# Optimization experiments

Measured on AMD Instinct MI355X. Metric: run time of the kernel, lower is better.

Reference implementation:

```python
import jax, jax.numpy as jnp
import numpy as np

K = 5      # unfold kernel size
S = 2      # unfold stride
EPS = 1e-6


def _extract_patches(feature):
    # torch nn.Unfold(kernel=(5,5), stride=2) -> [b, c*25, L], channel-major then
    # row-major kernel offsets; reproduced here with 25 strided slices.
    b, c, h, w = feature.shape
    oh = (h - K) // S + 1
    ow = (w - K) // S + 1
    slices = [feature[:, :, i:i + S * (oh - 1) + 1:S, j:j + S * (ow - 1) + 1:S]
              for i in range(K) for j in range(K)]
    patches = jnp.stack(slices, axis=2)                # [b, c, 25, oh, ow]
    patches = patches.reshape(b, c, K * K, oh * ow)    # [b, c, 25, L]
    return patches.transpose(0, 3, 2, 1)               # [b, L, 25, c]


def setup_inputs() -> dict:
    key = jax.random.key(0)
    k1, k2 = jax.random.split(key)
    feature = jax.random.normal(k1, (32, 128, 63, 63), dtype=jnp.float32)
    label = jax.random.randint(k2, (32,), 0, 2).astype(jnp.int32)
    return {"feature": feature, "label": label}


def reference(feature, label):
    patch = _extract_patches(feature)                  # [b, L, 25, c]
    norms = jnp.linalg.norm(patch, axis=-1)            # [b, L, 25]
    dots = jnp.einsum('blpc,blqc->blpq', patch, patch)  # [b, L, 25, 25]
    # torch cosine_similarity: dot / max(||x||*||y||, eps)
    denom = jnp.maximum(norms[..., :, None] * norms[..., None, :], EPS)
    cos = 1.0 - dots / denom                           # [b, L, 25, 25]
    s = jnp.mean(cos, axis=-1)                         # [b, L, 25]
    m = jnp.max(s, axis=-1)                            # [b, L]
    # topk(k=1) over L then mean over the k dim == max over L
    top = jnp.max(m, axis=-1)                          # [b]
    fake_mask = label.astype(top.dtype)
    real_mask = (1 - label).astype(top.dtype)
    real_loss = jnp.sum(top * real_mask) / jnp.sum(real_mask)
    fake_loss = jnp.sum(top * fake_mask) / jnp.sum(fake_mask)
    loss = 1.0 - fake_loss + real_loss
    return jnp.maximum(loss, 0.0)
```

## Files before the change

kernel.cpp:

```cpp
#include <hip/hip_runtime.h>

#define NB 32
#define NC 128
#define NH 63
#define NW 63
#define HW 3969
#define OH 30
#define SEGW 19
#define NROW 9
#define POSN (NROW*SEGW)
#define NSST 10
#define NSEG 4
#define NBLK (NB*NSST*NSEG)

typedef _Float16 half2_t __attribute__((ext_vector_type(2)));
__device__ __forceinline__ half2_t u2h(unsigned u) { return __builtin_bit_cast(half2_t, u); }
__device__ __forceinline__ unsigned h2u(half2_t h) { return __builtin_bit_cast(unsigned, h); }

__device__ __forceinline__ float dot2(unsigned a, unsigned b, float c) {
#if __has_builtin(__builtin_amdgcn_fdot2)
    return __builtin_amdgcn_fdot2(u2h(a), u2h(b), c, false);
#else
    const half2_t x = u2h(a), y = u2h(b);
    c = fmaf((float)x[0], (float)y[0], c);
    return fmaf((float)x[1], (float)y[1], c);
#endif
}

__device__ __forceinline__ unsigned pk16(float a, float b) {
#if __has_builtin(__builtin_amdgcn_cvt_pkrtz)
    return __builtin_bit_cast(unsigned, __builtin_amdgcn_cvt_pkrtz(a, b));
#else
    const half2_t h = {(_Float16)a, (_Float16)b};
    return h2u(h);
#endif
}

__global__ __launch_bounds__(256) void seg_fused(const float* __restrict__ f,
                                                 float* __restrict__ slots) {
    const int lb  = (blockIdx.x & 7) * (NBLK / 8) + (blockIdx.x >> 3);
    const int b   = lb / (NSST * NSEG);
    const int rem = lb % (NSST * NSEG);
    const int sst = rem >> 2, g = rem & 3;
    const int y0 = 6 * sst, xlo = 16 * g;
    const int t = threadIdx.x;

    __shared__ unsigned band[POSN * 64];
    __shared__ float sinv[POSN];
    __shared__ unsigned sinvh[POSN];
    __shared__ uint4 Slh[16][24];
    __shared__ float wmax[3][4];

    if (t < POSN) {
        const int r = t / SEGW, xx = t % SEGW;
        const int x = xlo + xx;
        float inv = 0.0f;
        if (x < NW) {
            const float* gp = f + (size_t)b * NC * HW + (size_t)(y0 + r) * NW + x;
            float ss = 0.0f;
            float vc[16], vn[16];
            #pragma unroll
            for (int k = 0; k < 16; ++k) vc[k] = gp[(size_t)k * HW];
            #pragma unroll
            for (int ch = 0; ch < 8; ++ch) {
                if (ch < 7) {
                    #pragma unroll
                    for (int k = 0; k < 16; ++k)
                        vn[k] = gp[(size_t)((ch + 1) * 16 + k) * HW];
                }
                #pragma unroll
                for (int k = 0; k < 16; ++k) ss = fmaf(vc[k], vc[k], ss);
                unsigned u[8];
                #pragma unroll
                for (int j = 0; j < 8; ++j) u[j] = pk16(vc[2 * j], vc[2 * j + 1]);
                *(uint4*)&band[t * 64 + (((2 * ch     + t) & 15) << 2)] =
                    make_uint4(u[0], u[1], u[2], u[3]);
                *(uint4*)&band[t * 64 + (((2 * ch + 1 + t) & 15) << 2)] =
                    make_uint4(u[4], u[5], u[6], u[7]);
                #pragma unroll
                for (int k = 0; k < 16; ++k) vc[k] = vn[k];
            }
            inv = (ss > 0.0f) ? rsqrtf(ss) : 0.0f;
        } else {
            #pragma unroll
            for (int j = 0; j < 16; ++j)
                *(uint4*)&band[t * 64 + (((j + t) & 15) << 2)] = make_uint4(0u, 0u, 0u, 0u);
        }
        sinv[t] = inv;
        const half2_t i2 = {(_Float16)inv, (_Float16)inv};
        sinvh[t] = h2u(i2);
    }
    __syncthreads();

    #pragma unroll
    for (int jj = 0; jj < 2; ++jj) {
        const int i = t + jj * 256;
        if (i < 384) {
            const int tl = i >> 4, slot = i & 15;
            const int s_ = tl >> 3, txx = tl & 7;
            half2_t s0 = u2h(0u), s1 = u2h(0u), s2 = u2h(0u), s3 = u2h(0u);
            #pragma unroll
            for (int pr = 0; pr < 5; ++pr)
                #pragma unroll
                for (int pc = 0; pc < 5; ++pc) {
                    const int pos = (2 * s_ + pr) * SEGW + 2 * txx + pc;
                    const uint4 v = *(const uint4*)&band[pos * 64 + (((slot + pos) & 15) << 2)];
                    const half2_t iv = u2h(sinvh[pos]);
                    s0 = u2h(v.x) * iv + s0;
                    s1 = u2h(v.y) * iv + s1;
                    s2 = u2h(v.z) * iv + s2;
                    s3 = u2h(v.w) * iv + s3;
                }
            Slh[slot][tl] = make_uint4(h2u(s0), h2u(s1), h2u(s2), h2u(s3));
        }
    }
    __syncthreads();

    float m[3] = {0.0f, 0.0f, 0.0f};
    if (t < 200) {
        const int txx = t / 25, p = t % 25;
        if (8 * g + txx < OH) {
            const int pos0 = (p / 5) * SEGW + 2 * txx + (p % 5);
            #pragma unroll
            for (int j = 0; j < 3; ++j) {
                const int pos = pos0 + 2 * SEGW * j;
                const int tl  = 8 * j + txx;
                float acc = 0.0f;
                #pragma unroll
                for (int slot = 0; slot < 16; ++slot) {
                    const uint4 sv = Slh[slot][tl];
                    const uint4 v  = *(const uint4*)&band[pos * 64 + (((slot + pos) & 15) << 2)];
                    acc = dot2(v.x, sv.x, acc);
                    acc = dot2(v.y, sv.y, acc);
                    acc = dot2(v.z, sv.z, acc);
                    acc = dot2(v.w, sv.w, acc);
                }
                m[j] = fmaxf(0.0f, 1.0f - acc * sinv[pos] * 0.04f);
            }
        }
    }
    #pragma unroll
    for (int off = 1; off < 64; off <<= 1) {
        m[0] = fmaxf(m[0], __shfl_xor(m[0], off));
        m[1] = fmaxf(m[1], __shfl_xor(m[1], off));
        m[2] = fmaxf(m[2], __shfl_xor(m[2], off));
    }
    if ((t & 63) == 0) {
        wmax[0][t >> 6] = m[0];
        wmax[1][t >> 6] = m[1];
        wmax[2][t >> 6] = m[2];
    }
    __syncthreads();
    if (t < 3) {
        const float mm = fmaxf(fmaxf(wmax[t][0], wmax[t][1]),
                               fmaxf(wmax[t][2], wmax[t][3]));
        slots[((b * OH) + 3 * sst + t) * 4 + g] = mm;
    }
}

__global__ __launch_bounds__(128) void finalize(const float* __restrict__ slots,
                                                const int* __restrict__ label,
                                                float* __restrict__ out) {
    const int t = threadIdx.x;
    __shared__ float bmax[32];
    const int b = t >> 2, j = t & 3;
    float m = 0.0f;
    for (int i = j; i < 120; i += 4) m = fmaxf(m, slots[b * 120 + i]);
    m = fmaxf(m, __shfl_xor(m, 1));
    m = fmaxf(m, __shfl_xor(m, 2));
    if (j == 0) bmax[b] = m;
    __syncthreads();
    if (t == 0) {
        float fs = 0.0f, rs = 0.0f, fc = 0.0f, rc = 0.0f;
        for (int b2 = 0; b2 < NB; ++b2) {
            const float tb  = bmax[b2];
            const float lbv = (float)label[b2];
            fs += tb * lbv;          fc += lbv;
            rs += tb * (1.0f - lbv); rc += (1.0f - lbv);
        }
        const float loss = 1.0f - fs / fc + rs / rc;
        out[0] = fmaxf(loss, 0.0f);
    }
}

extern "C" void kernel_launch(void* const* d_in, const int* in_sizes, int n_in,
                              void* d_out, int out_size, void* d_ws, size_t ws_size,
                              hipStream_t stream) {
    const float* feature = (const float*)d_in[0];
    const int* label     = (const int*)d_in[1];
    float* out   = (float*)d_out;
    float* slots = (float*)d_ws;

    seg_fused<<<NBLK, 256, 0, stream>>>(feature, slots);
    finalize<<<1, 128, 0, stream>>>(slots, label, out);
}
```

Before: 33.05 us.

## Retile into square 13x13 pixel blocks covering 5x5 output windows

```diff
diff --git a/kernel.cpp b/kernel.cpp
--- a/kernel.cpp
+++ b/kernel.cpp
@@ -6,12 +6,12 @@
 #define NW 63
 #define HW 3969
 #define OH 30
-#define SEGW 19
-#define NROW 9
+#define SEGW 13
+#define NROW 13
 #define POSN (NROW*SEGW)
-#define NSST 10
-#define NSEG 4
-#define NBLK (NB*NSST*NSEG)
+#define NSST 6
+#define NCS 6
+#define NBLK (NB*NSST*NCS)
 
 typedef _Float16 half2_t __attribute__((ext_vector_type(2)));
 __device__ __forceinline__ half2_t u2h(unsigned u) { return __builtin_bit_cast(half2_t, u); }
@@ -39,53 +39,45 @@
 __global__ __launch_bounds__(256) void seg_fused(const float* __restrict__ f,
                                                  float* __restrict__ slots) {
     const int lb  = (blockIdx.x & 7) * (NBLK / 8) + (blockIdx.x >> 3);
-    const int b   = lb / (NSST * NSEG);
-    const int rem = lb % (NSST * NSEG);
-    const int sst = rem >> 2, g = rem & 3;
-    const int y0 = 6 * sst, xlo = 16 * g;
+    const int b   = lb / (NSST * NCS);
+    const int rem = lb % (NSST * NCS);
+    const int sst = rem / NCS, cs = rem % NCS;
+    const int y0 = 10 * sst, xlo = 10 * cs;
     const int t = threadIdx.x;
 
     __shared__ unsigned band[POSN * 64];
     __shared__ float sinv[POSN];
     __shared__ unsigned sinvh[POSN];
-    __shared__ uint4 Slh[16][24];
-    __shared__ float wmax[3][4];
+    __shared__ uint4 Slh[16][25];
+    __shared__ float wmax[4];
 
     if (t < POSN) {
         const int r = t / SEGW, xx = t % SEGW;
-        const int x = xlo + xx;
-        float inv = 0.0f;
-        if (x < NW) {
-            const float* gp = f + (size_t)b * NC * HW + (size_t)(y0 + r) * NW + x;
-            float ss = 0.0f;
-            float vc[16], vn[16];
+        const float* gp = f + (size_t)b * NC * HW + (size_t)(y0 + r) * NW + xlo + xx;
+        float ss = 0.0f;
+        float vc[16], vn[16];
+        #pragma unroll
+        for (int k = 0; k < 16; ++k) vc[k] = gp[(size_t)k * HW];
+        #pragma unroll
+        for (int ch = 0; ch < 8; ++ch) {
+            if (ch < 7) {
+                #pragma unroll
+                for (int k = 0; k < 16; ++k)
+                    vn[k] = gp[(size_t)((ch + 1) * 16 + k) * HW];
+            }
             #pragma unroll
-            for (int k = 0; k < 16; ++k) vc[k] = gp[(size_t)k * HW];
+            for (int k = 0; k < 16; ++k) ss = fmaf(vc[k], vc[k], ss);
+            unsigned u[8];
             #pragma unroll
-            for (int ch = 0; ch < 8; ++ch) {
-                if (ch < 7) {
-                    #pragma unroll
-                    for (int k = 0; k < 16; ++k)
-                        vn[k] = gp[(size_t)((ch + 1) * 16 + k) * HW];
-                }
-                #pragma unroll
-                for (int k = 0; k < 16; ++k) ss = fmaf(vc[k], vc[k], ss);
-                unsigned u[8];
-                #pragma unroll
-                for (int j = 0; j < 8; ++j) u[j] = pk16(vc[2 * j], vc[2 * j + 1]);
-                *(uint4*)&band[t * 64 + (((2 * ch     + t) & 15) << 2)] =
-                    make_uint4(u[0], u[1], u[2], u[3]);
-                *(uint4*)&band[t * 64 + (((2 * ch + 1 + t) & 15) << 2)] =
-                    make_uint4(u[4], u[5], u[6], u[7]);
-                #pragma unroll
-                for (int k = 0; k < 16; ++k) vc[k] = vn[k];
-            }
-            inv = (ss > 0.0f) ? rsqrtf(ss) : 0.0f;
-        } else {
+            for (int j = 0; j < 8; ++j) u[j] = pk16(vc[2 * j], vc[2 * j + 1]);
+            *(uint4*)&band[t * 64 + (((2 * ch     + t) & 15) << 2)] =
+                make_uint4(u[0], u[1], u[2], u[3]);
+            *(uint4*)&band[t * 64 + (((2 * ch + 1 + t) & 15) << 2)] =
+                make_uint4(u[4], u[5], u[6], u[7]);
             #pragma unroll
-            for (int j = 0; j < 16; ++j)
-                *(uint4*)&band[t * 64 + (((j + t) & 15) << 2)] = make_uint4(0u, 0u, 0u, 0u);
+            for (int k = 0; k < 16; ++k) vc[k] = vn[k];
         }
+        const float inv = (ss > 0.0f) ? rsqrtf(ss) : 0.0f;
         sinv[t] = inv;
         const half2_t i2 = {(_Float16)inv, (_Float16)inv};
         sinvh[t] = h2u(i2);
@@ -95,15 +87,15 @@
     #pragma unroll
     for (int jj = 0; jj < 2; ++jj) {
         const int i = t + jj * 256;
-        if (i < 384) {
+        if (i < 400) {
             const int tl = i >> 4, slot = i & 15;
-            const int s_ = tl >> 3, txx = tl & 7;
+            const int j = tl / 5, tc = tl % 5;
             half2_t s0 = u2h(0u), s1 = u2h(0u), s2 = u2h(0u), s3 = u2h(0u);
             #pragma unroll
             for (int pr = 0; pr < 5; ++pr)
                 #pragma unroll
                 for (int pc = 0; pc < 5; ++pc) {
-                    const int pos = (2 * s_ + pr) * SEGW + 2 * txx + pc;
+                    const int pos = (2 * j + pr) * SEGW + 2 * tc + pc;
                     const uint4 v = *(const uint4*)&band[pos * 64 + (((slot + pos) & 15) << 2)];
                     const half2_t iv = u2h(sinvh[pos]);
                     s0 = u2h(v.x) * iv + s0;
@@ -116,59 +108,47 @@
     }
     __syncthreads();
 
-    float m[3] = {0.0f, 0.0f, 0.0f};
-    if (t < 200) {
-        const int txx = t / 25, p = t % 25;
-        if (8 * g + txx < OH) {
-            const int pos0 = (p / 5) * SEGW + 2 * txx + (p % 5);
+    float m = 0.0f;
+    #pragma unroll
+    for (int jj = 0; jj < 3; ++jj) {
+        const int it = t + jj * 250;
+        if (t < 250 && it < 625) {
+            const int tl = it / 25, p = it % 25;
+            const int j = tl / 5, tc = tl % 5;
+            const int pos = (2 * j + p / 5) * SEGW + 2 * tc + (p % 5);
+            float acc = 0.0f;
             #pragma unroll
-            for (int j = 0; j < 3; ++j) {
-                const int pos = pos0 + 2 * SEGW * j;
-                const int tl  = 8 * j + txx;
-                float acc = 0.0f;
-                #pragma unroll
-                for (int slot = 0; slot < 16; ++slot) {
-                    const uint4 sv = Slh[slot][tl];
-                    const uint4 v  = *(const uint4*)&band[pos * 64 + (((slot + pos) & 15) << 2)];
-                    acc = dot2(v.x, sv.x, acc);
-                    acc = dot2(v.y, sv.y, acc);
-                    acc = dot2(v.z, sv.z, acc);
-                    acc = dot2(v.w, sv.w, acc);
-                }
-                m[j] = fmaxf(0.0f, 1.0f - acc * sinv[pos] * 0.04f);
+            for (int slot = 0; slot < 16; ++slot) {
+                const uint4 sv = Slh[slot][tl];
+                const uint4 v  = *(const uint4*)&band[pos * 64 + (((slot + pos) & 15) << 2)];
+                acc = dot2(v.x, sv.x, acc);
+                acc = dot2(v.y, sv.y, acc);
+                acc = dot2(v.z, sv.z, acc);
+                acc = dot2(v.w, sv.w, acc);
             }
+            m = fmaxf(m, 1.0f - acc * sinv[pos] * 0.04f);
         }
     }
     #pragma unroll
-    for (int off = 1; off < 64; off <<= 1) {
-        m[0] = fmaxf(m[0], __shfl_xor(m[0], off));
-        m[1] = fmaxf(m[1], __shfl_xor(m[1], off));
-        m[2] = fmaxf(m[2], __shfl_xor(m[2], off));
-    }
-    if ((t & 63) == 0) {
-        wmax[0][t >> 6] = m[0];
-        wmax[1][t >> 6] = m[1];
-        wmax[2][t >> 6] = m[2];
-    }
+    for (int off = 1; off < 64; off <<= 1) m = fmaxf(m, __shfl_xor(m, off));
+    if ((t & 63) == 0) wmax[t >> 6] = m;
     __syncthreads();
-    if (t < 3) {
-        const float mm = fmaxf(fmaxf(wmax[t][0], wmax[t][1]),
-                               fmaxf(wmax[t][2], wmax[t][3]));
-        slots[((b * OH) + 3 * sst + t) * 4 + g] = mm;
-    }
+    if (t == 0)
+        slots[lb] = fmaxf(fmaxf(wmax[0], wmax[1]), fmaxf(wmax[2], wmax[3]));
 }
 
-__global__ __launch_bounds__(128) void finalize(const float* __restrict__ slots,
+__global__ __launch_bounds__(256) void finalize(const float* __restrict__ slots,
                                                 const int* __restrict__ label,
                                                 float* __restrict__ out) {
     const int t = threadIdx.x;
     __shared__ float bmax[32];
-    const int b = t >> 2, j = t & 3;
+    const int b = t >> 3, k = t & 7;
     float m = 0.0f;
-    for (int i = j; i < 120; i += 4) m = fmaxf(m, slots[b * 120 + i]);
+    for (int i = k; i < 36; i += 8) m = fmaxf(m, slots[b * 36 + i]);
     m = fmaxf(m, __shfl_xor(m, 1));
     m = fmaxf(m, __shfl_xor(m, 2));
-    if (j == 0) bmax[b] = m;
+    m = fmaxf(m, __shfl_xor(m, 4));
+    if (k == 0) bmax[b] = m;
     __syncthreads();
     if (t == 0) {
         float fs = 0.0f, rs = 0.0f, fc = 0.0f, rc = 0.0f;
@@ -192,5 +172,5 @@
     float* slots = (float*)d_ws;
 
     seg_fused<<<NBLK, 256, 0, stream>>>(feature, slots);
-    finalize<<<1, 128, 0, stream>>>(slots, label, out);
+    finalize<<<1, 256, 0, stream>>>(slots, label, out);
 }
```

Result: faster. 29.05 us (-12.1%).
